# Optimization experiments

Hardware: AMD Instinct MI355X
Metric: run time of the kernel (lower is better)

Reference implementation:

```python
import jax, jax.numpy as jnp
import numpy as np


def setup_inputs() -> dict:
    key = jax.random.key(0)
    k1, k2 = jax.random.split(key)
    B, Q, P, D = 4, 75, 5, 640  # episodes, queries, prototypes (5-way), feat dim (ResNet-12)
    return {
        "query_feat": jax.random.normal(k1, (B, Q, D), dtype=jnp.float32),
        "proto_feat": jax.random.normal(k2, (B, P, D), dtype=jnp.float32),
    }


def reference(query_feat, proto_feat):
    # Kendall rank correlation (default mode of ProtoLayer).
    # c_pair = combinations(range(D), 2); x[:, c_pair].diff(-1).sign() ==
    # sign(x[..., j] - x[..., i]) for all i < j.
    D = query_feat.shape[-1]
    i_idx, j_idx = np.triu_indices(D, k=1)  # same order as itertools.combinations
    n_pairs = i_idx.shape[0]  # D*(D-1)/2
    q_rank = jnp.sign(query_feat[..., j_idx] - query_feat[..., i_idx])  # (B, Q, n_pairs)
    s_rank = jnp.sign(proto_feat[..., j_idx] - proto_feat[..., i_idx])  # (B, P, n_pairs)
    # per-batch: query_prank @ support_prank.T / n_pairs -> (B, Q, P)
    return jnp.einsum("bqn,bpn->bqp", q_rank, s_rank) / n_pairs
```

## Files before the change

kernel.cpp:

```cpp
#include <hip/hip_runtime.h>
#include <stdint.h>


#define BB 4
#define QQ 75
#define PP 5
#define DD 640
#define NPAIRS 204480
#define NGROUPS 110
#define NROWS_P 20
#define GPW 5

__device__ __forceinline__ unsigned pack_word(const float* __restrict__ xi,
                                              float xj, int dlo, int lane) {
    unsigned w = 0;
#pragma unroll
    for (int t = 0; t < 32; ++t)
        w = (w << 1) | (xi[t] < xj ? 1u : 0u);
    if (dlo >= 0) {
        const int n = lane - dlo;
        const unsigned msk = (n <= 0) ? 0u
                           : (n >= 32) ? 0xFFFFFFFFu
                                       : (0xFFFFFFFFu << (32 - n));
        w &= msk;
    }
    return w;
}

__device__ __forceinline__ unsigned wave_sum(unsigned v) {
#pragma unroll
    for (int o = 32; o > 0; o >>= 1) v += __shfl_xor((int)v, o, 64);
    return v;
}

__global__ __launch_bounds__(256, 4)
void pack_p(const float* __restrict__ pfeat, unsigned* __restrict__ pm) {
    const int lane = threadIdx.x & 63;
    const int wave = __builtin_amdgcn_readfirstlane(threadIdx.x >> 6);
    const int rp   = blockIdx.x;
    const int G    = blockIdx.y * 4 + wave;
    if (G >= NGROUPS) return;

    int gj = 0;
#pragma unroll 1
    while ((gj + 1) * (gj + 2) <= G) ++gj;
    const int ig = G - gj * (gj + 1);

    const float* __restrict__ row = pfeat + (size_t)rp * DD;
    const float xj = row[64 * gj + lane];
    pm[((size_t)G * NROWS_P + rp) * 64 + lane] =
        pack_word(row + 32 * ig, xj, 32 * ig - 64 * gj, lane);
}

__global__ __launch_bounds__(256, 4)
void kendall(const float* __restrict__ qfeat,
             const unsigned* __restrict__ pm,
             float* __restrict__ out) {
    const int lane = threadIdx.x & 63;
    const int wave = __builtin_amdgcn_readfirstlane(threadIdx.x >> 6);
    const int bq   = blockIdx.x;
    const int slot = blockIdx.y * 4 + wave;
    if (slot >= NGROUPS / GPW) return;
    const int b    = bq / QQ;
    const float* __restrict__ row = qfeat + (size_t)bq * DD;

    unsigned m0 = 0, m1 = 0, m2 = 0, m3 = 0, m4 = 0;

    const int G0 = GPW * slot;
    int gj = 0;
#pragma unroll 1
    while ((gj + 1) * (gj + 2) <= G0) ++gj;
    int ig = G0 - gj * (gj + 1);

#pragma unroll 1
    for (int k = 0; k < GPW; ++k) {
        const int G = G0 + k;
        const float xj = row[64 * gj + lane];
        const unsigned qw =
            pack_word(row + 32 * ig, xj, 32 * ig - 64 * gj, lane);
        const unsigned* __restrict__ pr =
            pm + ((size_t)G * NROWS_P + b * PP) * 64 + lane;
        m0 += __popc(qw ^ pr[0]);
        m1 += __popc(qw ^ pr[64]);
        m2 += __popc(qw ^ pr[128]);
        m3 += __popc(qw ^ pr[192]);
        m4 += __popc(qw ^ pr[256]);
        if (++ig == 2 * gj + 2) { ++gj; ig = 0; }
    }

    unsigned c01 = wave_sum(m0 | (m1 << 16));
    unsigned c23 = wave_sum(m2 | (m3 << 16));
    unsigned c4  = wave_sum(m4);

    if (lane == 0) {
        const float base = (slot == 0) ? 1.0f : 0.0f;
        const float s = -2.0f / (float)NPAIRS;
        float* o = out + (size_t)bq * PP;
        atomicAdd(o + 0, base + s * (float)(c01 & 0xFFFFu));
        atomicAdd(o + 1, base + s * (float)(c01 >> 16));
        atomicAdd(o + 2, base + s * (float)(c23 & 0xFFFFu));
        atomicAdd(o + 3, base + s * (float)(c23 >> 16));
        atomicAdd(o + 4, base + s * (float)c4);
    }
}

extern "C" void kernel_launch(void* const* d_in, const int* in_sizes, int n_in,
                              void* d_out, int out_size, void* d_ws, size_t ws_size,
                              hipStream_t stream) {
    const float* qfeat = (const float*)d_in[0];
    const float* pfeat = (const float*)d_in[1];
    float* out = (float*)d_out;
    unsigned* pm = (unsigned*)d_ws;

    pack_p <<<dim3(NROWS_P, 28), 256, 0, stream>>>(pfeat, pm);
    kendall<<<dim3(BB * QQ, 6),  256, 0, stream>>>(qfeat, pm, out);
}
```

Before: 70.50 us.

## Fuse prototype packing into Kendall kernel with LDS-shared prototype words

Merges the two launches into one kernel. Each block handles one episode and a slot of two pair-groups: it first packs the prototype sign words into shared memory, then loops its waves over the 75 queries, reusing the prototype words held in registers. This removes the workspace round-trip and the second launch's overhead, and shares prototype packing across queries. In exchange the grid becomes 4x55 blocks of 512 threads and there are many more atomic adds per output element, one per slot.

```diff
diff --git a/kernel.cpp b/kernel.cpp
--- a/kernel.cpp
+++ b/kernel.cpp
@@ -8,8 +8,9 @@
 #define DD 640
 #define NPAIRS 204480
 #define NGROUPS 110
-#define NROWS_P 20
-#define GPW 5
+#define GPW 2
+#define NSLOT (NGROUPS / GPW)
+#define WPB 8
 
 __device__ __forceinline__ unsigned pack_word(const float* __restrict__ xi,
                                               float xj, int dlo, int lane) {
@@ -33,74 +34,80 @@
     return v;
 }
 
-__global__ __launch_bounds__(256, 4)
-void pack_p(const float* __restrict__ pfeat, unsigned* __restrict__ pm) {
+__global__ __launch_bounds__(512, 2)
+void kendall_fused(const float* __restrict__ qfeat,
+                   const float* __restrict__ pfeat,
+                   float* __restrict__ out) {
+    __shared__ unsigned plds[GPW * PP * 64];
+
     const int lane = threadIdx.x & 63;
     const int wave = __builtin_amdgcn_readfirstlane(threadIdx.x >> 6);
-    const int rp   = blockIdx.x;
-    const int G    = blockIdx.y * 4 + wave;
-    if (G >= NGROUPS) return;
+    const int b    = blockIdx.x;
+    const int slot = blockIdx.y;
+    const int G0   = GPW * slot;
 
-    int gj = 0;
+    int gj0 = 0;
 #pragma unroll 1
-    while ((gj + 1) * (gj + 2) <= G) ++gj;
-    const int ig = G - gj * (gj + 1);
+    while ((gj0 + 1) * (gj0 + 2) <= G0) ++gj0;
+    const int ig0 = G0 - gj0 * (gj0 + 1);
+    int gj1 = gj0, ig1 = ig0 + 1;
+    if (ig1 == 2 * gj1 + 2) { ++gj1; ig1 = 0; }
+    const int dlo0 = 32 * ig0 - 64 * gj0;
+    const int dlo1 = 32 * ig1 - 64 * gj1;
 
-    const float* __restrict__ row = pfeat + (size_t)rp * DD;
-    const float xj = row[64 * gj + lane];
-    pm[((size_t)G * NROWS_P + rp) * 64 + lane] =
-        pack_word(row + 32 * ig, xj, 32 * ig - 64 * gj, lane);
-}
+    const float* __restrict__ pbase = pfeat + (size_t)b * PP * DD;
+#pragma unroll 1
+    for (int widx = wave; widx < GPW * PP; widx += WPB) {
+        const int g   = (widx >= PP) ? 1 : 0;
+        const int row = widx - g * PP;
+        const int gj  = g ? gj1 : gj0;
+        const int ig  = g ? ig1 : ig0;
+        const int dlo = g ? dlo1 : dlo0;
+        const float* __restrict__ prow = pbase + (size_t)row * DD;
+        plds[widx * 64 + lane] =
+            pack_word(prow + 32 * ig, prow[64 * gj + lane], dlo, lane);
+    }
+    __syncthreads();
 
-__global__ __launch_bounds__(256, 4)
-void kendall(const float* __restrict__ qfeat,
-             const unsigned* __restrict__ pm,
-             float* __restrict__ out) {
-    const int lane = threadIdx.x & 63;
-    const int wave = __builtin_amdgcn_readfirstlane(threadIdx.x >> 6);
-    const int bq   = blockIdx.x;
-    const int slot = blockIdx.y * 4 + wave;
-    if (slot >= NGROUPS / GPW) return;
-    const int b    = bq / QQ;
-    const float* __restrict__ row = qfeat + (size_t)bq * DD;
-
-    unsigned m0 = 0, m1 = 0, m2 = 0, m3 = 0, m4 = 0;
-
-    const int G0 = GPW * slot;
-    int gj = 0;
-#pragma unroll 1
-    while ((gj + 1) * (gj + 2) <= G0) ++gj;
-    int ig = G0 - gj * (gj + 1);
+    const unsigned pw00 = plds[(0 * PP + 0) * 64 + lane];
+    const unsigned pw01 = plds[(0 * PP + 1) * 64 + lane];
+    const unsigned pw02 = plds[(0 * PP + 2) * 64 + lane];
+    const unsigned pw03 = plds[(0 * PP + 3) * 64 + lane];
+    const unsigned pw04 = plds[(0 * PP + 4) * 64 + lane];
+    const unsigned pw10 = plds[(1 * PP + 0) * 64 + lane];
+    const unsigned pw11 = plds[(1 * PP + 1) * 64 + lane];
+    const unsigned pw12 = plds[(1 * PP + 2) * 64 + lane];
+    const unsigned pw13 = plds[(1 * PP + 3) * 64 + lane];
+    const unsigned pw14 = plds[(1 * PP + 4) * 64 + lane];
 
 #pragma unroll 1
-    for (int k = 0; k < GPW; ++k) {
-        const int G = G0 + k;
-        const float xj = row[64 * gj + lane];
-        const unsigned qw =
-            pack_word(row + 32 * ig, xj, 32 * ig - 64 * gj, lane);
-        const unsigned* __restrict__ pr =
-            pm + ((size_t)G * NROWS_P + b * PP) * 64 + lane;
-        m0 += __popc(qw ^ pr[0]);
-        m1 += __popc(qw ^ pr[64]);
-        m2 += __popc(qw ^ pr[128]);
-        m3 += __popc(qw ^ pr[192]);
-        m4 += __popc(qw ^ pr[256]);
-        if (++ig == 2 * gj + 2) { ++gj; ig = 0; }
-    }
+    for (int r = wave; r < QQ; r += WPB) {
+        const int bq = b * QQ + r;
+        const float* __restrict__ qrow = qfeat + (size_t)bq * DD;
+        const unsigned q0 =
+            pack_word(qrow + 32 * ig0, qrow[64 * gj0 + lane], dlo0, lane);
+        const unsigned q1 =
+            pack_word(qrow + 32 * ig1, qrow[64 * gj1 + lane], dlo1, lane);
+        const unsigned m0 = __popc(q0 ^ pw00) + __popc(q1 ^ pw10);
+        const unsigned m1 = __popc(q0 ^ pw01) + __popc(q1 ^ pw11);
+        const unsigned m2 = __popc(q0 ^ pw02) + __popc(q1 ^ pw12);
+        const unsigned m3 = __popc(q0 ^ pw03) + __popc(q1 ^ pw13);
+        const unsigned m4 = __popc(q0 ^ pw04) + __popc(q1 ^ pw14);
 
-    unsigned c01 = wave_sum(m0 | (m1 << 16));
-    unsigned c23 = wave_sum(m2 | (m3 << 16));
-    unsigned c4  = wave_sum(m4);
+        const unsigned c01 = wave_sum(m0 | (m1 << 16));
+        const unsigned c23 = wave_sum(m2 | (m3 << 16));
+        const unsigned c4  = wave_sum(m4);
 
-    if (lane == 0) {
-        const float base = (slot == 0) ? 1.0f : 0.0f;
-        const float s = -2.0f / (float)NPAIRS;
-        float* o = out + (size_t)bq * PP;
-        atomicAdd(o + 0, base + s * (float)(c01 & 0xFFFFu));
-        atomicAdd(o + 1, base + s * (float)(c01 >> 16));
-        atomicAdd(o + 2, base + s * (float)(c23 & 0xFFFFu));
-        atomicAdd(o + 3, base + s * (float)(c23 >> 16));
-        atomicAdd(o + 4, base + s * (float)c4);
+        if (lane == 0) {
+            const float base = (slot == 0) ? 1.0f : 0.0f;
+            const float s = -2.0f / (float)NPAIRS;
+            float* o = out + (size_t)bq * PP;
+            atomicAdd(o + 0, base + s * (float)(c01 & 0xFFFFu));
+            atomicAdd(o + 1, base + s * (float)(c01 >> 16));
+            atomicAdd(o + 2, base + s * (float)(c23 & 0xFFFFu));
+            atomicAdd(o + 3, base + s * (float)(c23 >> 16));
+            atomicAdd(o + 4, base + s * (float)c4);
+        }
     }
 }
 
@@ -110,8 +117,7 @@
     const float* qfeat = (const float*)d_in[0];
     const float* pfeat = (const float*)d_in[1];
     float* out = (float*)d_out;
-    unsigned* pm = (unsigned*)d_ws;
+    (void)d_ws; (void)ws_size;
 
-    pack_p <<<dim3(NROWS_P, 28), 256, 0, stream>>>(pfeat, pm);
-    kendall<<<dim3(BB * QQ, 6),  256, 0, stream>>>(qfeat, pm, out);
+    kendall_fused<<<dim3(BB, NSLOT), 512, 0, stream>>>(qfeat, pfeat, out);
 }
```

New measurement: 116.8 us. 65.7% more time.
